# Kernel tuning notes

Measured on AMD Instinct MI355X. Metric: run time of the kernel, lower is better.

Reference implementation:

```python
import jax, jax.numpy as jnp
import numpy as np

D_MODEL = 1024
NHEAD = 16
HEAD_DIM = D_MODEL // NHEAD
D_FF = 4096
EPS = 1e-5


def _linear(x, w, b):
    # torch Linear: y = x @ W^T + b, W is [out, in]
    return x @ w.T + b


def _layernorm(x, g, b):
    mu = jnp.mean(x, axis=-1, keepdims=True)
    var = jnp.var(x, axis=-1, keepdims=True)
    return (x - mu) * jax.lax.rsqrt(var + EPS) * g + b


def setup_inputs() -> dict:
    key = jax.random.key(0)
    ks = jax.random.split(key, 16)
    s = 0.02
    inp = {
        'x': jax.random.normal(ks[0], (2048, D_MODEL), jnp.float32),
        'q_in_w': s * jax.random.normal(ks[1], (D_MODEL, D_MODEL), jnp.float32),
        'q_in_b': jnp.zeros((D_MODEL,), jnp.float32),
        'k_in_w': s * jax.random.normal(ks[2], (D_MODEL, D_MODEL), jnp.float32),
        'k_in_b': jnp.zeros((D_MODEL,), jnp.float32),
        'v_in_w': s * jax.random.normal(ks[3], (D_MODEL, D_MODEL), jnp.float32),
        'v_in_b': jnp.zeros((D_MODEL,), jnp.float32),
        'out_w': s * jax.random.normal(ks[4], (D_MODEL, D_MODEL), jnp.float32),
        'out_b': jnp.zeros((D_MODEL,), jnp.float32),
        'ffn1_w': s * jax.random.normal(ks[5], (D_FF, D_MODEL), jnp.float32),
        'ffn1_b': jnp.zeros((D_FF,), jnp.float32),
        'ffn2_w': s * jax.random.normal(ks[6], (D_MODEL, D_FF), jnp.float32),
        'ffn2_b': jnp.zeros((D_MODEL,), jnp.float32),
        'n1_g': jnp.ones((D_MODEL,), jnp.float32),
        'n1_b': jnp.zeros((D_MODEL,), jnp.float32),
        'n2_g': jnp.ones((D_MODEL,), jnp.float32),
        'n2_b': jnp.zeros((D_MODEL,), jnp.float32),
        'q_out_w': s * jax.random.normal(ks[7], (D_MODEL, D_MODEL), jnp.float32),
        'q_out_b': jnp.zeros((D_MODEL,), jnp.float32),
        'k_out_w': s * jax.random.normal(ks[8], (D_MODEL, D_MODEL), jnp.float32),
        'k_out_b': jnp.zeros((D_MODEL,), jnp.float32),
        'v_out_w': s * jax.random.normal(ks[9], (D_MODEL, D_MODEL), jnp.float32),
        'v_out_b': jnp.zeros((D_MODEL,), jnp.float32),
        'seq_length': 2048,
    }
    return inp


def reference(x, q_in_w, q_in_b, k_in_w, k_in_b, v_in_w, v_in_b,
              out_w, out_b, ffn1_w, ffn1_b, ffn2_w, ffn2_b,
              n1_g, n1_b, n2_g, n2_b,
              q_out_w, q_out_b, k_out_w, k_out_b, v_out_w, v_out_b,
              seq_length):
    S = seq_length
    # --- is_first: batched in-projections (replaces per-token loop + cat) ---
    q_buf = _linear(x, q_in_w, q_in_b)   # [S, D]
    k_buf = _linear(x, k_in_w, k_in_b)
    v_buf = _linear(x, v_in_w, v_in_b)
    prev_layer_input = x

    # --- multi-head attention (non-causal, no mask) ---
    q = q_buf.reshape(S, NHEAD, HEAD_DIM).transpose(1, 0, 2)  # [H, S, Dh]
    k = k_buf.reshape(S, NHEAD, HEAD_DIM).transpose(1, 0, 2)
    v = v_buf.reshape(S, NHEAD, HEAD_DIM).transpose(1, 0, 2)
    scale = 1.0 / np.sqrt(HEAD_DIM).astype(np.float32)
    scores = jnp.einsum('hqd,hkd->hqk', q, k) * scale        # [H, S, S]
    attn = jax.nn.softmax(scores, axis=-1)
    ctx = jnp.einsum('hqk,hkd->hqd', attn, v)                # [H, S, Dh]
    attn_output = ctx.transpose(1, 0, 2).reshape(S, D_MODEL)  # [S, D]

    # --- post-norm residual blocks (batched over tokens) ---
    h = _linear(attn_output, out_w, out_b)
    h = _layernorm(prev_layer_input + h, n1_g, n1_b)
    ff = _linear(jax.nn.relu(_linear(h, ffn1_w, ffn1_b)), ffn2_w, ffn2_b)
    y = _layernorm(h + ff, n2_g, n2_b)                        # [S, D]

    # --- not is_last: out-projections for the next layer ---
    q_next = _linear(y, q_out_w, q_out_b)
    k_next = _linear(y, k_out_w, k_out_b)
    v_next = _linear(y, v_out_w, v_out_b)
    return (q_next, k_next, v_next, y)
```

## Files before the change

### kernel.cpp

```cpp
#include <hip/hip_runtime.h>
#include <math.h>

#define SEQ   2048
#define DM    1024
#define NH    16
#define DH    64
#define DFF   4096
#define KVSPLIT 4

typedef __bf16 bf16;
using bf16x8 = __attribute__((ext_vector_type(8))) __bf16;
using bf16x4 = __attribute__((ext_vector_type(4))) __bf16;
using f32x4  = __attribute__((ext_vector_type(4))) float;

__device__ __forceinline__ unsigned short f2bfu(float f) {
    unsigned int u = __float_as_uint(f);
    u += 0x7FFF + ((u >> 16) & 1);
    return (unsigned short)(u >> 16);
}
__device__ __forceinline__ bf16 f2bf(float f) {
    unsigned short s = f2bfu(f);
    return __builtin_bit_cast(bf16, s);
}

__device__ __forceinline__ unsigned cvt_pk_bf16(float lo, float hi) {
    unsigned r;
    asm("v_cvt_pk_bf16_f32 %0, %1, %2" : "=v"(r) : "v"(lo), "v"(hi));
    return r;
}

__device__ __forceinline__ void gll16(const bf16* g, bf16* lds_base) {
    __builtin_amdgcn_global_load_lds(
        (const __attribute__((address_space(1))) unsigned int*)g,
        (__attribute__((address_space(3))) unsigned int*)lds_base, 16, 0, 0);
}

__device__ __forceinline__ int xcd_swz(int wid, int nwg) {
    return (wid & 7) * (nwg >> 3) + (wid >> 3);
}

__global__ __launch_bounds__(256) void conv_k(const float* __restrict__ src,
                                              bf16* __restrict__ dst, int n) {
    int i = (blockIdx.x * 256 + threadIdx.x) * 4;
    if (i >= n) return;
    float4 v = *(const float4*)(src + i);
    ushort4 o;
    o.x = f2bfu(v.x); o.y = f2bfu(v.y); o.z = f2bfu(v.z); o.w = f2bfu(v.w);
    *(ushort4*)((unsigned short*)dst + i) = o;
}

struct ConvSeg  { const float* src; bf16* dst; int n; };
struct ConvSegs { ConvSeg s[6]; };

__global__ __launch_bounds__(256) void conv_multi_k(ConvSegs cs) {
    ConvSeg sg = cs.s[blockIdx.y];
    int i = (blockIdx.x * 256 + threadIdx.x) * 4;
    if (i >= sg.n) return;
    float4 v = *(const float4*)(sg.src + i);
    ushort4 o;
    o.x = f2bfu(v.x); o.y = f2bfu(v.y); o.z = f2bfu(v.z); o.w = f2bfu(v.w);
    *(ushort4*)((unsigned short*)sg.dst + i) = o;
}

struct GemmPtrs {
    const bf16* W[3];
    const float* bias[3];
    float* out32[3];
    bf16*  out16[3];
    float scale[3];
};

template<int BM, int BN, int BK>
__global__ __launch_bounds__(256) void gemm_bf16_k(
    const bf16* __restrict__ A, GemmPtrs p, int N, int K, int relu)
{
    constexpr int TM = BM / 32;
    constexpr int TN = BN / 32;
    constexpr int KK = BK / 32;
    constexpr int CH = BK / 8;
    __shared__ bf16 As[BM][BK];
    __shared__ bf16 Ws[BN][BK];

    const int t    = threadIdx.x;
    const int lane = t & 63;
    const int wave = t >> 6;
    const int quad = lane >> 4;
    const int l15  = lane & 15;
    const int wm   = (wave >> 1) * (BM / 2);
    const int wn   = (wave & 1) * (BN / 2);
    const int m0   = blockIdx.y * BM;
    const int n0   = blockIdx.x * BN;
    const int xm   = l15 & (CH - 1);
    const bf16* __restrict__ W = p.W[blockIdx.z];

    f32x4 acc[TM][TN];
    #pragma unroll
    for (int i = 0; i < TM; ++i)
        #pragma unroll
        for (int j = 0; j < TN; ++j)
            acc[i][j] = f32x4{0.f, 0.f, 0.f, 0.f};

    for (int k0 = 0; k0 < K; k0 += BK) {
        #pragma unroll
        for (int s = 0; s < BM * BK / 2048; ++s) {
            int base = s * 256 + wave * 64;
            int idx  = base + lane;
            int row  = idx / CH;
            int c    = idx % CH;
            gll16(A + (long)(m0 + row) * K + k0 + ((c ^ (row & (CH - 1))) * 8),
                  &As[0][0] + (long)base * 8);
        }
        #pragma unroll
        for (int s = 0; s < BN * BK / 2048; ++s) {
            int base = s * 256 + wave * 64;
            int idx  = base + lane;
            int row  = idx / CH;
            int c    = idx % CH;
            gll16(W + (long)(n0 + row) * K + k0 + ((c ^ (row & (CH - 1))) * 8),
                  &Ws[0][0] + (long)base * 8);
        }
        __syncthreads();

        bf16x8 a[TM][KK], b[TN][KK];
        #pragma unroll
        for (int i = 0; i < TM; ++i)
            #pragma unroll
            for (int kk = 0; kk < KK; ++kk)
                a[i][kk] = *(const bf16x8*)
                    &As[wm + i * 16 + l15][((kk * 4 + quad) ^ xm) * 8];
        #pragma unroll
        for (int j = 0; j < TN; ++j)
            #pragma unroll
            for (int kk = 0; kk < KK; ++kk)
                b[j][kk] = *(const bf16x8*)
                    &Ws[wn + j * 16 + l15][((kk * 4 + quad) ^ xm) * 8];
        #pragma unroll
        for (int kk = 0; kk < KK; ++kk)
            #pragma unroll
            for (int i = 0; i < TM; ++i)
                #pragma unroll
                for (int j = 0; j < TN; ++j)
                    acc[i][j] = __builtin_amdgcn_mfma_f32_16x16x32_bf16(
                        a[i][kk], b[j][kk], acc[i][j], 0, 0, 0);
        __syncthreads();
    }

    float* o32 = p.out32[blockIdx.z];
    bf16*  o16 = p.out16[blockIdx.z];
    const float* bias = p.bias[blockIdx.z];
    const float scl = p.scale[blockIdx.z];
    #pragma unroll
    for (int j = 0; j < TN; ++j) {
        int n = n0 + wn + j * 16 + l15;
        float bv = bias[n];
        #pragma unroll
        for (int i = 0; i < TM; ++i) {
            #pragma unroll
            for (int r = 0; r < 4; ++r) {
                int m = m0 + wm + i * 16 + quad * 4 + r;
                float v = (acc[i][j][r] + bv) * scl;
                if (relu) v = fmaxf(v, 0.f);
                if (o32) o32[(long)m * N + n] = v;
                if (o16) o16[(long)m * N + n] = f2bf(v);
            }
        }
    }
}

template<int BM, int BN, int BK, int KS>
__global__ __launch_bounds__(256) void gemm_splitk_k(
    const bf16* __restrict__ A, const bf16* __restrict__ W,
    float* __restrict__ part, int N, int K)
{
    constexpr int TM = BM / 32;
    constexpr int TN = BN / 32;
    constexpr int KK = BK / 32;
    constexpr int CH = BK / 8;
    __shared__ bf16 As[BM][BK];
    __shared__ bf16 Ws[BN][BK];

    const int t    = threadIdx.x;
    const int lane = t & 63;
    const int wave = t >> 6;
    const int quad = lane >> 4;
    const int l15  = lane & 15;
    const int wm   = (wave >> 1) * (BM / 2);
    const int wn   = (wave & 1) * (BN / 2);
    const int m0   = blockIdx.y * BM;
    const int n0   = blockIdx.x * BN;
    const int xm   = l15 & (CH - 1);
    const int Kp   = K / KS;
    const int klo  = blockIdx.z * Kp;
    const long MN  = (long)gridDim.y * BM * N;

    f32x4 acc[TM][TN];
    #pragma unroll
    for (int i = 0; i < TM; ++i)
        #pragma unroll
        for (int j = 0; j < TN; ++j)
            acc[i][j] = f32x4{0.f, 0.f, 0.f, 0.f};

    for (int k0 = klo; k0 < klo + Kp; k0 += BK) {
        #pragma unroll
        for (int s = 0; s < BM * BK / 2048; ++s) {
            int base = s * 256 + wave * 64;
            int idx  = base + lane;
            int row  = idx / CH;
            int c    = idx % CH;
            gll16(A + (long)(m0 + row) * K + k0 + ((c ^ (row & (CH - 1))) * 8),
                  &As[0][0] + (long)base * 8);
        }
        #pragma unroll
        for (int s = 0; s < BN * BK / 2048; ++s) {
            int base = s * 256 + wave * 64;
            int idx  = base + lane;
            int row  = idx / CH;
            int c    = idx % CH;
            gll16(W + (long)(n0 + row) * K + k0 + ((c ^ (row & (CH - 1))) * 8),
                  &Ws[0][0] + (long)base * 8);
        }
        __syncthreads();

        bf16x8 a[TM][KK], b[TN][KK];
        #pragma unroll
        for (int i = 0; i < TM; ++i)
            #pragma unroll
            for (int kk = 0; kk < KK; ++kk)
                a[i][kk] = *(const bf16x8*)
                    &As[wm + i * 16 + l15][((kk * 4 + quad) ^ xm) * 8];
        #pragma unroll
        for (int j = 0; j < TN; ++j)
            #pragma unroll
            for (int kk = 0; kk < KK; ++kk)
                b[j][kk] = *(const bf16x8*)
                    &Ws[wn + j * 16 + l15][((kk * 4 + quad) ^ xm) * 8];
        #pragma unroll
        for (int kk = 0; kk < KK; ++kk)
            #pragma unroll
            for (int i = 0; i < TM; ++i)
                #pragma unroll
                for (int j = 0; j < TN; ++j)
                    acc[i][j] = __builtin_amdgcn_mfma_f32_16x16x32_bf16(
                        a[i][kk], b[j][kk], acc[i][j], 0, 0, 0);
        __syncthreads();
    }

    float* o = part + (long)blockIdx.z * MN;
    #pragma unroll
    for (int j = 0; j < TN; ++j) {
        int n = n0 + wn + j * 16 + l15;
        #pragma unroll
        for (int i = 0; i < TM; ++i)
            #pragma unroll
            for (int r = 0; r < 4; ++r) {
                int m = m0 + wm + i * 16 + quad * 4 + r;
                o[(long)m * N + n] = acc[i][j][r];
            }
    }
}

__global__ __launch_bounds__(256) void attn_mfma_k(
    const bf16* __restrict__ Q, const bf16* __restrict__ Kg,
    const bf16* __restrict__ Vg, bf16* __restrict__ Opart,
    float* __restrict__ lpart)
{
    __shared__ bf16 Kb[64][64];
    __shared__ bf16 Vt[64][72];

    const int nwg = gridDim.x * gridDim.y * gridDim.z;
    const int wid = blockIdx.x + gridDim.x * (blockIdx.y + gridDim.y * blockIdx.z);
    const int sw  = xcd_swz(wid, nwg);
    const int bx  = sw % gridDim.x;
    const int rem = sw / gridDim.x;
    const int h   = rem % gridDim.y;
    const int spl = rem / gridDim.y;
    const int q0  = bx * 64;

    const int t    = threadIdx.x;
    const int lane = t & 63;
    const int wave = t >> 6;
    const int quad = lane >> 4;
    const int l15  = lane & 15;
    const int cb   = h * DH;
    const long SD  = (long)SEQ * DM;

    const int qrow = q0 + wave * 16 + l15;
    bf16x8 bQ[2];
    #pragma unroll
    for (int kh = 0; kh < 2; ++kh)
        bQ[kh] = *(const bf16x8*)(Q + (long)qrow * DM + cb + kh * 32 + quad * 8);

    f32x4 o_acc[4];
    #pragma unroll
    for (int dt = 0; dt < 4; ++dt) o_acc[dt] = f32x4{0.f, 0.f, 0.f, 0.f};
    float lsum = 0.f;

    const int kv_lo = spl * (SEQ / KVSPLIT);
    const int kv_hi = kv_lo + SEQ / KVSPLIT;

    for (int kv0 = kv_lo; kv0 < kv_hi; kv0 += 64) {
        __syncthreads();
        #pragma unroll
        for (int s = 0; s < 2; ++s) {
            int idx = s * 256 + t;
            int row = idx >> 3;
            int dg  = idx & 7;
            gll16(Kg + (long)(kv0 + row) * DM + cb + ((dg ^ (row & 7)) * 8),
                  &Kb[0][0] + (s * 256 + wave * 64) * 8);
        }
        #pragma unroll
        for (int s = 0; s < 2; ++s) {
            int i  = t + s * 256;
            int h4 = (i & 1) * 4;
            int dg = (i >> 1) & 7;
            int kp = i >> 4;
            int k0 = ((kp & 16) << 1) | (kp & 15);
            const bf16* vb = Vg + (long)(kv0 + k0) * DM + cb + dg * 8 + h4;
            bf16x4 a0 = *(const bf16x4*)vb;
            bf16x4 a1 = *(const bf16x4*)(vb + 16 * DM);
            int vk0 = (k0 & 32) | ((k0 & 15) << 1);
            int col = vk0 ^ (dg * 8);
            int d0  = dg * 8 + h4;
            #pragma unroll
            for (int j = 0; j < 4; ++j) {
                unsigned lo = __builtin_bit_cast(unsigned short, a0[j]);
                unsigned hi = __builtin_bit_cast(unsigned short, a1[j]);
                *(unsigned*)&Vt[d0 + j][col] = lo | (hi << 16);
            }
        }
        __syncthreads();

        float p[16];
        #pragma unroll
        for (int kt = 0; kt < 4; ++kt) {
            int krow = kt * 16 + l15;
            bf16x8 a0 = *(const bf16x8*)&Kb[krow][(quad ^ (l15 & 7)) * 8];
            bf16x8 a1 = *(const bf16x8*)&Kb[krow][((4 + quad) ^ (l15 & 7)) * 8];
            f32x4 sv = f32x4{0.f, 0.f, 0.f, 0.f};
            sv = __builtin_amdgcn_mfma_f32_16x16x32_bf16(a0, bQ[0], sv, 0, 0, 0);
            sv = __builtin_amdgcn_mfma_f32_16x16x32_bf16(a1, bQ[1], sv, 0, 0, 0);
            #pragma unroll
            for (int r = 0; r < 4; ++r) p[kt * 4 + r] = exp2f(sv[r]);
        }

        #pragma unroll
        for (int i = 0; i < 16; ++i) lsum += p[i];

        bf16x8 aP[2];
        #pragma unroll
        for (int c = 0; c < 2; ++c) {
            union { unsigned u[4]; bf16x8 v; } pk;
            #pragma unroll
            for (int w4 = 0; w4 < 4; ++w4)
                pk.u[w4] = cvt_pk_bf16(p[c * 8 + w4], p[c * 8 + 4 + w4]);
            aP[c] = pk.v;
        }

        #pragma unroll
        for (int dt = 0; dt < 4; ++dt) {
            int d   = dt * 16 + l15;
            int dgr = d >> 3;
            bf16x8 v0 = *(const bf16x8*)&Vt[d][(quad ^ dgr) * 8];
            bf16x8 v1 = *(const bf16x8*)&Vt[d][((4 + quad) ^ dgr) * 8];
            o_acc[dt] = __builtin_amdgcn_mfma_f32_16x16x32_bf16(aP[0], v0, o_acc[dt], 0, 0, 0);
            o_acc[dt] = __builtin_amdgcn_mfma_f32_16x16x32_bf16(aP[1], v1, o_acc[dt], 0, 0, 0);
        }
    }

    #pragma unroll
    for (int r = 0; r < 4; ++r) {
        int row = q0 + wave * 16 + quad * 4 + r;
        #pragma unroll
        for (int dt = 0; dt < 4; ++dt)
            Opart[(long)spl * SD + (long)row * DM + cb + dt * 16 + l15] =
                f2bf(o_acc[dt][r]);
    }
    lsum += __shfl_xor(lsum, 16);
    lsum += __shfl_xor(lsum, 32);
    if (quad == 0)
        lpart[((long)spl * NH + h) * SEQ + qrow] = lsum;
}

__global__ __launch_bounds__(256) void attn_reduce_k(
    const bf16* __restrict__ Opart, const float* __restrict__ lpart,
    bf16* __restrict__ O)
{
    const long SD = (long)SEQ * DM;
    long i = ((long)blockIdx.x * 256 + threadIdx.x) * 8;
    int row = (int)(i / DM);
    int h   = (int)((i % DM) / DH);

    float l = 0.f;
    #pragma unroll
    for (int k = 0; k < KVSPLIT; ++k)
        l += lpart[((long)k * NH + h) * SEQ + row];
    float inv = 1.f / l;

    float acc[8] = {};
    #pragma unroll
    for (int k = 0; k < KVSPLIT; ++k) {
        bf16x8 v = *(const bf16x8*)(Opart + (long)k * SD + i);
        #pragma unroll
        for (int j = 0; j < 8; ++j) acc[j] += (float)v[j];
    }
    bf16x8 o;
    #pragma unroll
    for (int j = 0; j < 8; ++j) o[j] = f2bf(acc[j] * inv);
    *(bf16x8*)(O + i) = o;
}

template<int NS>
__global__ __launch_bounds__(256) void ln_red_k(
    const float* __restrict__ part, const float* __restrict__ bias,
    const float* __restrict__ res, const float* __restrict__ g,
    const float* __restrict__ b, float* __restrict__ out32,
    bf16* __restrict__ out16)
{
    const long SD = (long)SEQ * DM;
    const int row = blockIdx.x;
    const int t   = threadIdx.x;
    const long off = (long)row * DM + (t << 2);

    float4 v = *(const float4*)(res + off);
    float4 bv0 = *(const float4*)(bias + (t << 2));
    v.x += bv0.x; v.y += bv0.y; v.z += bv0.z; v.w += bv0.w;
    #pragma unroll
    for (int z = 0; z < NS; ++z) {
        float4 pz = *(const float4*)(part + z * SD + off);
        v.x += pz.x; v.y += pz.y; v.z += pz.z; v.w += pz.w;
    }

    float s1 = v.x + v.y + v.z + v.w;
    float s2 = v.x * v.x + v.y * v.y + v.z * v.z + v.w * v.w;
    #pragma unroll
    for (int off2 = 32; off2 > 0; off2 >>= 1) {
        s1 += __shfl_xor(s1, off2);
        s2 += __shfl_xor(s2, off2);
    }
    __shared__ float red[8];
    int wid = t >> 6, lid = t & 63;
    if (lid == 0) { red[wid] = s1; red[4 + wid] = s2; }
    __syncthreads();
    s1 = red[0] + red[1] + red[2] + red[3];
    s2 = red[4] + red[5] + red[6] + red[7];

    float mu   = s1 * (1.f / DM);
    float var  = s2 * (1.f / DM) - mu * mu;
    float rstd = rsqrtf(var + 1e-5f);

    float4 gv = *(const float4*)(g + (t << 2));
    float4 bv = *(const float4*)(b + (t << 2));
    float4 ov;
    ov.x = (v.x - mu) * rstd * gv.x + bv.x;
    ov.y = (v.y - mu) * rstd * gv.y + bv.y;
    ov.z = (v.z - mu) * rstd * gv.z + bv.z;
    ov.w = (v.w - mu) * rstd * gv.w + bv.w;
    if (out32) *(float4*)(out32 + off) = ov;
    if (out16) {
        ushort4 o;
        o.x = f2bfu(ov.x); o.y = f2bfu(ov.y); o.z = f2bfu(ov.z); o.w = f2bfu(ov.w);
        *(ushort4*)((unsigned short*)out16 + off) = o;
    }
}

extern "C" void kernel_launch(void* const* d_in, const int* in_sizes, int n_in,
                              void* d_out, int out_size, void* d_ws, size_t ws_size,
                              hipStream_t stream)
{
    const float* x       = (const float*)d_in[0];
    const float* q_in_w  = (const float*)d_in[1];
    const float* q_in_b  = (const float*)d_in[2];
    const float* k_in_w  = (const float*)d_in[3];
    const float* k_in_b  = (const float*)d_in[4];
    const float* v_in_w  = (const float*)d_in[5];
    const float* v_in_b  = (const float*)d_in[6];
    const float* out_w   = (const float*)d_in[7];
    const float* out_b   = (const float*)d_in[8];
    const float* ffn1_w  = (const float*)d_in[9];
    const float* ffn1_b  = (const float*)d_in[10];
    const float* ffn2_w  = (const float*)d_in[11];
    const float* ffn2_b  = (const float*)d_in[12];
    const float* n1_g    = (const float*)d_in[13];
    const float* n1_b    = (const float*)d_in[14];
    const float* n2_g    = (const float*)d_in[15];
    const float* n2_b    = (const float*)d_in[16];
    const float* q_out_w = (const float*)d_in[17];
    const float* q_out_b = (const float*)d_in[18];
    const float* k_out_w = (const float*)d_in[19];
    const float* k_out_b = (const float*)d_in[20];
    const float* v_out_w = (const float*)d_in[21];
    const float* v_out_b = (const float*)d_in[22];

    float* out = (float*)d_out;
    const long SD = (long)SEQ * DM;
    const long MB = 1024 * 1024;

    char* w = (char*)d_ws;
    bf16*  xbf   = (bf16*)(w);
    float* lpart = (float*)(w);
    bf16*  qb    = (bf16*)(w + 4  * MB);
    bf16*  kb    = (bf16*)(w + 8  * MB);
    bf16*  vb    = (bf16*)(w + 12 * MB);
    bf16*  atnb  = (bf16*)(w + 16 * MB);
    float* h32   = (float*)(w);
    bf16*  h16   = (bf16*)(w + 8  * MB);
    float* P2    = (float*)(w + 8  * MB);
    bf16*  Opart = (bf16*)(w + 20 * MB);
    float* P1    = (float*)(w + 20 * MB);
    bf16*  f1    = (bf16*)(w + 24 * MB);
    bf16*  wqi   = (bf16*)(w + 32 * MB);
    bf16*  wki   = (bf16*)(w + 34 * MB);
    bf16*  wvi   = (bf16*)(w + 36 * MB);
    bf16*  wo    = (bf16*)(w + 38 * MB);
    bf16*  wf1   = (bf16*)(w + 40 * MB);
    bf16*  wf2   = (bf16*)(w + 40 * MB);
    bf16*  wqo   = (bf16*)(w + 24 * MB);
    bf16*  wko   = (bf16*)(w + 26 * MB);
    bf16*  wvo   = (bf16*)(w + 28 * MB);
    bf16*  ybf   = (bf16*)(w + 30 * MB);
    float* y32   = out + 3 * SD;

    dim3 blk(256);
    const int DD = DM * DM;
    const float SCL = 0.18033688f;

    {
        ConvSegs cs;
        cs.s[0] = {x,      xbf, (int)SD};
        cs.s[1] = {q_in_w, wqi, DD};
        cs.s[2] = {k_in_w, wki, DD};
        cs.s[3] = {v_in_w, wvi, DD};
        cs.s[4] = {out_w,  wo,  DD};
        cs.s[5] = {ffn1_w, wf1, DM * DFF};
        conv_multi_k<<<dim3(DM * DFF / 1024, 6), blk, 0, stream>>>(cs);
    }

    {
        GemmPtrs p{};
        p.W[0] = wqi; p.W[1] = wki; p.W[2] = wvi;
        p.bias[0] = q_in_b; p.bias[1] = k_in_b; p.bias[2] = v_in_b;
        p.out16[0] = qb; p.out16[1] = kb; p.out16[2] = vb;
        p.scale[0] = SCL; p.scale[1] = 1.0f; p.scale[2] = 1.0f;
        gemm_bf16_k<128, 64, 64><<<dim3(DM / 64, SEQ / 128, 3), blk, 0, stream>>>(
            xbf, p, DM, DM, 0);
    }

    attn_mfma_k<<<dim3(SEQ / 64, NH, KVSPLIT), blk, 0, stream>>>(
        qb, kb, vb, Opart, lpart);
    attn_reduce_k<<<dim3((int)(SD / 2048)), blk, 0, stream>>>(Opart, lpart, atnb);

    gemm_splitk_k<64, 128, 64, 2><<<dim3(DM / 128, SEQ / 64, 2), blk, 0, stream>>>(
        atnb, wo, P1, DM, DM);

    ln_red_k<2><<<SEQ, blk, 0, stream>>>(P1, out_b, x, n1_g, n1_b, h32, h16);

    {
        GemmPtrs p{};
        p.W[0] = wf1; p.bias[0] = ffn1_b; p.out16[0] = f1;
        p.scale[0] = 1.0f; p.scale[1] = 1.0f; p.scale[2] = 1.0f;
        gemm_bf16_k<128, 128, 64><<<dim3(DFF / 128, SEQ / 128, 1), blk, 0, stream>>>(
            h16, p, DFF, DM, 1);
    }

    conv_k<<<dim3(DM * DFF / 1024), blk, 0, stream>>>(ffn2_w, wf2, DM * DFF);

    gemm_splitk_k<64, 128, 64, 2><<<dim3(DM / 128, SEQ / 64, 2), blk, 0, stream>>>(
        f1, wf2, P2, DM, DFF);

    {
        ConvSegs cs;
        cs.s[0] = {q_out_w, wqo, DD};
        cs.s[1] = {k_out_w, wko, DD};
        cs.s[2] = {v_out_w, wvo, DD};
        cs.s[3] = cs.s[0]; cs.s[4] = cs.s[0]; cs.s[5] = cs.s[0];
        conv_multi_k<<<dim3(DD / 1024, 3), blk, 0, stream>>>(cs);
    }

    ln_red_k<2><<<SEQ, blk, 0, stream>>>(P2, ffn2_b, h32, n2_g, n2_b, y32, ybf);

    {
        GemmPtrs p{};
        p.W[0] = wqo; p.W[1] = wko; p.W[2] = wvo;
        p.bias[0] = q_out_b; p.bias[1] = k_out_b; p.bias[2] = v_out_b;
        p.out32[0] = out; p.out32[1] = out + SD; p.out32[2] = out + 2 * SD;
        p.scale[0] = 1.0f; p.scale[1] = 1.0f; p.scale[2] = 1.0f;
        gemm_bf16_k<128, 64, 64><<<dim3(DM / 64, SEQ / 128, 3), blk, 0, stream>>>(
            ybf, p, DM, DM, 0);
    }
}
```

Before: 324.8 us.

## Double-buffer LDS tiles in GEMM kernels to overlap global loads with MFMA

Both GEMM kernels now keep two LDS buffers per operand and prefetch the next K tile with async global-to-LDS loads while MFMAs run on the current one. Explicit vmcnt waits and raw s_barrier replace the __syncthreads pairs, so load latency is meant to hide behind compute. LDS use doubles, which can lower occupancy, and the hand-written waitcnt count must match the number of loads issued per stage.

```diff
diff --git a/kernel.cpp b/kernel.cpp
--- a/kernel.cpp
+++ b/kernel.cpp
@@ -74,12 +74,13 @@
 __global__ __launch_bounds__(256) void gemm_bf16_k(
     const bf16* __restrict__ A, GemmPtrs p, int N, int K, int relu)
 {
-    constexpr int TM = BM / 32;
-    constexpr int TN = BN / 32;
-    constexpr int KK = BK / 32;
-    constexpr int CH = BK / 8;
-    __shared__ bf16 As[BM][BK];
-    __shared__ bf16 Ws[BN][BK];
+    constexpr int TM  = BM / 32;
+    constexpr int TN  = BN / 32;
+    constexpr int KK  = BK / 32;
+    constexpr int CH  = BK / 8;
+    constexpr int LPS = (BM + BN) * BK / 2048;
+    __shared__ bf16 As[2][BM][BK];
+    __shared__ bf16 Ws[2][BN][BK];
 
     const int t    = threadIdx.x;
     const int lane = t & 63;
@@ -100,7 +101,7 @@
         for (int j = 0; j < TN; ++j)
             acc[i][j] = f32x4{0.f, 0.f, 0.f, 0.f};
 
-    for (int k0 = 0; k0 < K; k0 += BK) {
+    auto stage = [&](int buf, int k0) {
         #pragma unroll
         for (int s = 0; s < BM * BK / 2048; ++s) {
             int base = s * 256 + wave * 64;
@@ -108,7 +109,7 @@
             int row  = idx / CH;
             int c    = idx % CH;
             gll16(A + (long)(m0 + row) * K + k0 + ((c ^ (row & (CH - 1))) * 8),
-                  &As[0][0] + (long)base * 8);
+                  &As[buf][0][0] + (long)base * 8);
         }
         #pragma unroll
         for (int s = 0; s < BN * BK / 2048; ++s) {
@@ -117,9 +118,21 @@
             int row  = idx / CH;
             int c    = idx % CH;
             gll16(W + (long)(n0 + row) * K + k0 + ((c ^ (row & (CH - 1))) * 8),
-                  &Ws[0][0] + (long)base * 8);
-        }
-        __syncthreads();
+                  &Ws[buf][0][0] + (long)base * 8);
+        }
+    };
+
+    stage(0, 0);
+    int cur = 0;
+    for (int k0 = 0; k0 < K; k0 += BK) {
+        if (k0 + BK < K) {
+            stage(cur ^ 1, k0 + BK);
+            asm volatile("s_waitcnt vmcnt(%0)" :: "i"(LPS) : "memory");
+        } else {
+            asm volatile("s_waitcnt vmcnt(0)" ::: "memory");
+        }
+        __builtin_amdgcn_s_barrier();
+        __builtin_amdgcn_sched_barrier(0);
 
         bf16x8 a[TM][KK], b[TN][KK];
         #pragma unroll
@@ -127,13 +140,13 @@
             #pragma unroll
             for (int kk = 0; kk < KK; ++kk)
                 a[i][kk] = *(const bf16x8*)
-                    &As[wm + i * 16 + l15][((kk * 4 + quad) ^ xm) * 8];
+                    &As[cur][wm + i * 16 + l15][((kk * 4 + quad) ^ xm) * 8];
         #pragma unroll
         for (int j = 0; j < TN; ++j)
             #pragma unroll
             for (int kk = 0; kk < KK; ++kk)
                 b[j][kk] = *(const bf16x8*)
-                    &Ws[wn + j * 16 + l15][((kk * 4 + quad) ^ xm) * 8];
+                    &Ws[cur][wn + j * 16 + l15][((kk * 4 + quad) ^ xm) * 8];
         #pragma unroll
         for (int kk = 0; kk < KK; ++kk)
             #pragma unroll
@@ -142,7 +155,10 @@
                 for (int j = 0; j < TN; ++j)
                     acc[i][j] = __builtin_amdgcn_mfma_f32_16x16x32_bf16(
                         a[i][kk], b[j][kk], acc[i][j], 0, 0, 0);
-        __syncthreads();
+
+        __builtin_amdgcn_sched_barrier(0);
+        __builtin_amdgcn_s_barrier();
+        cur ^= 1;
     }
 
     float* o32 = p.out32[blockIdx.z];
@@ -172,12 +188,13 @@
     const bf16* __restrict__ A, const bf16* __restrict__ W,
     float* __restrict__ part, int N, int K)
 {
-    constexpr int TM = BM / 32;
-    constexpr int TN = BN / 32;
-    constexpr int KK = BK / 32;
-    constexpr int CH = BK / 8;
-    __shared__ bf16 As[BM][BK];
-    __shared__ bf16 Ws[BN][BK];
+    constexpr int TM  = BM / 32;
+    constexpr int TN  = BN / 32;
+    constexpr int KK  = BK / 32;
+    constexpr int CH  = BK / 8;
+    constexpr int LPS = (BM + BN) * BK / 2048;
+    __shared__ bf16 As[2][BM][BK];
+    __shared__ bf16 Ws[2][BN][BK];
 
     const int t    = threadIdx.x;
     const int lane = t & 63;
@@ -200,7 +217,7 @@
         for (int j = 0; j < TN; ++j)
             acc[i][j] = f32x4{0.f, 0.f, 0.f, 0.f};
 
-    for (int k0 = klo; k0 < klo + Kp; k0 += BK) {
+    auto stage = [&](int buf, int k0) {
         #pragma unroll
         for (int s = 0; s < BM * BK / 2048; ++s) {
             int base = s * 256 + wave * 64;
@@ -208,7 +225,7 @@
             int row  = idx / CH;
             int c    = idx % CH;
             gll16(A + (long)(m0 + row) * K + k0 + ((c ^ (row & (CH - 1))) * 8),
-                  &As[0][0] + (long)base * 8);
+                  &As[buf][0][0] + (long)base * 8);
         }
         #pragma unroll
         for (int s = 0; s < BN * BK / 2048; ++s) {
@@ -217,9 +234,21 @@
             int row  = idx / CH;
             int c    = idx % CH;
             gll16(W + (long)(n0 + row) * K + k0 + ((c ^ (row & (CH - 1))) * 8),
-                  &Ws[0][0] + (long)base * 8);
-        }
-        __syncthreads();
+                  &Ws[buf][0][0] + (long)base * 8);
+        }
+    };
+
+    stage(0, klo);
+    int cur = 0;
+    for (int k0 = klo; k0 < klo + Kp; k0 += BK) {
+        if (k0 + BK < klo + Kp) {
+            stage(cur ^ 1, k0 + BK);
+            asm volatile("s_waitcnt vmcnt(%0)" :: "i"(LPS) : "memory");
+        } else {
+            asm volatile("s_waitcnt vmcnt(0)" ::: "memory");
+        }
+        __builtin_amdgcn_s_barrier();
+        __builtin_amdgcn_sched_barrier(0);
 
         bf16x8 a[TM][KK], b[TN][KK];
         #pragma unroll
@@ -227,13 +256,13 @@
             #pragma unroll
             for (int kk = 0; kk < KK; ++kk)
                 a[i][kk] = *(const bf16x8*)
-                    &As[wm + i * 16 + l15][((kk * 4 + quad) ^ xm) * 8];
+                    &As[cur][wm + i * 16 + l15][((kk * 4 + quad) ^ xm) * 8];
         #pragma unroll
         for (int j = 0; j < TN; ++j)
             #pragma unroll
             for (int kk = 0; kk < KK; ++kk)
                 b[j][kk] = *(const bf16x8*)
-                    &Ws[wn + j * 16 + l15][((kk * 4 + quad) ^ xm) * 8];
+                    &Ws[cur][wn + j * 16 + l15][((kk * 4 + quad) ^ xm) * 8];
         #pragma unroll
         for (int kk = 0; kk < KK; ++kk)
             #pragma unroll
@@ -242,7 +271,10 @@
                 for (int j = 0; j < TN; ++j)
                     acc[i][j] = __builtin_amdgcn_mfma_f32_16x16x32_bf16(
                         a[i][kk], b[j][kk], acc[i][j], 0, 0, 0);
-        __syncthreads();
+
+        __builtin_amdgcn_sched_barrier(0);
+        __builtin_amdgcn_s_barrier();
+        cur ^= 1;
     }
 
     float* o = part + (long)blockIdx.z * MN;
```

Result: no change. 321.5 us (-1.0%).
